# Optimization experiments

Hardware: AMD Instinct MI355X
Metric: run time of the kernel (lower is better)

## Reference

```python
import jax, jax.numpy as jnp
import numpy as np

N_RAYS = 131072
N_NODES = 524288
ENC_DEPTH = 8
ENC_DIM = 16
N_POINTS = 8
IN_DIM = N_POINTS * ENC_DEPTH * ENC_DIM  # 1024
INNER = 64


def setup_inputs() -> dict:
    key = jax.random.key(0)
    ks = jax.random.split(key, 9)
    orig = jax.random.uniform(ks[0], (N_RAYS, 3), dtype=jnp.float32)
    end = jax.random.uniform(ks[1], (N_RAYS, 3), dtype=jnp.float32)
    history = jax.random.randint(ks[2], (N_RAYS, ENC_DEPTH), 0, N_NODES, dtype=jnp.int32).astype(jnp.int64)
    nodes_min = jax.random.uniform(ks[3], (N_NODES, 3), dtype=jnp.float32)
    # extents strictly positive (module replaces 0 extents with 0.5)
    nodes_extent = jax.random.uniform(ks[4], (N_NODES, 3), dtype=jnp.float32) + 0.1
    emb = jax.random.normal(ks[5], (N_NODES, 8 * ENC_DIM), dtype=jnp.float32) * 0.1
    W1 = jax.random.normal(ks[6], (IN_DIM, INNER), dtype=jnp.float32) * (1.0 / np.sqrt(IN_DIM))
    W2 = jax.random.normal(ks[7], (INNER, INNER), dtype=jnp.float32) * (1.0 / np.sqrt(INNER))
    W3 = jax.random.normal(ks[8], (INNER, 2), dtype=jnp.float32) * (1.0 / np.sqrt(INNER))
    return {"orig": orig, "end": end, "history": history, "nodes_min": nodes_min,
            "nodes_extent": nodes_extent, "emb": emb, "W1": W1, "W2": W2, "W3": W3}


def _net_forward(orig, end, history, nodes_min, nodes_extent, emb, W1, W2, W3):
    n = orig.shape[0]
    d = history.shape[1]
    # gather per-ray, per-depth node data (irregular access)
    nmin = nodes_min[history]          # (n, d, 3)
    ext = nodes_extent[history]        # (n, d, 3)
    po = jnp.clip((orig[:, None, :] - nmin) / ext, 0.0, 1.0)  # (n, d, 3)
    pe = jnp.clip((end[:, None, :] - nmin) / ext, 0.0, 1.0)
    ts = jnp.linspace(0.0, 1.0, N_POINTS, dtype=orig.dtype)
    pts = po[:, :, None, :] + (pe - po)[:, :, None, :] * ts[None, None, :, None]  # (n, d, P, 3)
    xd, yd, zd = pts[..., 0], pts[..., 1], pts[..., 2]
    # corner weights in the same order as bbox_feature.chunk(8): 000,100,010,001,101,011,110,111
    w = jnp.stack([
        (1 - xd) * (1 - yd) * (1 - zd),
        xd * (1 - yd) * (1 - zd),
        (1 - xd) * yd * (1 - zd),
        (1 - xd) * (1 - yd) * zd,
        xd * (1 - yd) * zd,
        (1 - xd) * yd * zd,
        xd * yd * (1 - zd),
        xd * yd * zd,
    ], axis=-1)                                    # (n, d, P, 8)
    corners = emb[history].reshape(n, d, 8, ENC_DIM)  # (n, d, 8, F)
    feat = jnp.einsum('ndpk,ndkf->ndpf', w, corners)  # (n, d, P, F)
    feat = feat.reshape(n, d * N_POINTS * ENC_DIM)    # concat over depth
    h = jax.nn.relu(feat @ W1)
    h = jax.nn.relu(h @ W2)
    a = h @ W3                                        # (n, 2)
    lengths = jnp.linalg.norm(end - orig, axis=-1)
    pred_cls = a[:, 0]
    pred_dist = a[:, 1] * lengths
    return jnp.stack([pred_cls, pred_dist], axis=-1)  # (n, 2)


def reference(orig, end, history, nodes_min, nodes_extent, emb, W1, W2, W3):
    return _net_forward(orig, end, history, nodes_min, nodes_extent, emb, W1, W2, W3)
```

## Files before the change

### kernel.cpp

```cpp
#include <hip/hip_runtime.h>
#include <hip/hip_bf16.h>
#include <cstdint>

#define ENC_DEPTH 8
#define RAYS_PER_BLOCK 64
#define THREADS 512

typedef __attribute__((ext_vector_type(8))) short bf16x8;
typedef __attribute__((ext_vector_type(4))) float f32x4;

__device__ __forceinline__ unsigned short f2bf(float x) {
    union { float f; unsigned u; } v; v.f = x;
    unsigned r = v.u + 0x7fffu + ((v.u >> 16) & 1u);
    return (unsigned short)(r >> 16);
}
__device__ __forceinline__ float bf2f(unsigned short h) {
    union { unsigned u; float f; } v; v.u = ((unsigned)h) << 16;
    return v.f;
}
__device__ __forceinline__ float clamp01(float x) {
    return fminf(fmaxf(x, 0.0f), 1.0f);
}

__global__ __launch_bounds__(THREADS, 4) void nbvh_kernel(
    const float* __restrict__ orig, const float* __restrict__ endp,
    const int* __restrict__ hist, const float* __restrict__ nodes_min,
    const float* __restrict__ nodes_extent, const float* __restrict__ emb,
    const float* __restrict__ W1, const float* __restrict__ W2,
    const float* __restrict__ W3, float* __restrict__ out)
{
    __shared__ int hist_s[RAYS_PER_BLOCK * ENC_DEPTH];
    __shared__ float oe_s[RAYS_PER_BLOCK * 6];
    __shared__ __align__(16) unsigned short corners_s[RAYS_PER_BLOCK * 136];
    __shared__ __align__(16) unsigned short feat_s[RAYS_PER_BLOCK * 144];
    __shared__ __align__(16) unsigned short w1t_s[64 * 144];
    __shared__ float h1_s[RAYS_PER_BLOCK * 65];

    const int t = threadIdx.x;
    const int r0 = blockIdx.x * RAYS_PER_BLOCK;
    const int wave = t >> 6;
    const int lane = t & 63;

    hist_s[t] = hist[r0 * ENC_DEPTH + t];
    if (t < RAYS_PER_BLOCK * 3) {
        int ray = t / 3, c = t - ray * 3;
        oe_s[ray * 6 + c]     = orig[(r0 + ray) * 3 + c];
        oe_s[ray * 6 + 3 + c] = endp[(r0 + ray) * 3 + c];
    }

    f32x4 acc0 = {0.f, 0.f, 0.f, 0.f};
    f32x4 acc1 = {0.f, 0.f, 0.f, 0.f};
    const int m0 = (wave >> 1) * 16;
    const int n0 = (wave & 1) * 32;

    __syncthreads();

    for (int d = 0; d < ENC_DEPTH; ++d) {
        {
            int ray = t >> 3, k = t & 7;
            int node = hist_s[(ray << 3) + d];
            const float4* ep = (const float4*)(emb + ((size_t)node << 7) + (k << 4));
            float4 e0 = ep[0], e1 = ep[1], e2 = ep[2], e3 = ep[3];
            float e[16];
            e[0]=e0.x; e[1]=e0.y; e[2]=e0.z; e[3]=e0.w;
            e[4]=e1.x; e[5]=e1.y; e[6]=e1.z; e[7]=e1.w;
            e[8]=e2.x; e[9]=e2.y; e[10]=e2.z; e[11]=e2.w;
            e[12]=e3.x; e[13]=e3.y; e[14]=e3.z; e[15]=e3.w;
            unsigned short* cb = corners_s + ray * 136 + k;
            #pragma unroll
            for (int f = 0; f < 16; ++f) cb[f << 3] = f2bf(e[f]);
        }
        {
            int rl = t >> 2, cg = (t & 3) << 4;
            const float4* wp = (const float4*)(W1 + (size_t)(d * 128 + rl) * 64 + cg);
            float4 a0v = wp[0], a1v = wp[1], a2v = wp[2], a3v = wp[3];
            float a[16];
            a[0]=a0v.x; a[1]=a0v.y; a[2]=a0v.z; a[3]=a0v.w;
            a[4]=a1v.x; a[5]=a1v.y; a[6]=a1v.z; a[7]=a1v.w;
            a[8]=a2v.x; a[9]=a2v.y; a[10]=a2v.z; a[11]=a2v.w;
            a[12]=a3v.x; a[13]=a3v.y; a[14]=a3v.z; a[15]=a3v.w;
            unsigned short* wb = w1t_s + (size_t)cg * 144 + rl;
            #pragma unroll
            for (int i = 0; i < 16; ++i) wb[i * 144] = f2bf(a[i]);
        }
        __syncthreads();

        {
            int ray = t >> 3, p = t & 7;
            int node = hist_s[(ray << 3) + d];
            float nm0 = nodes_min[node * 3 + 0];
            float nm1 = nodes_min[node * 3 + 1];
            float nm2 = nodes_min[node * 3 + 2];
            float ex0 = nodes_extent[node * 3 + 0];
            float ex1 = nodes_extent[node * 3 + 1];
            float ex2 = nodes_extent[node * 3 + 2];
            const float* oe = oe_s + ray * 6;
            float po0 = clamp01((oe[0] - nm0) / ex0);
            float po1 = clamp01((oe[1] - nm1) / ex1);
            float po2 = clamp01((oe[2] - nm2) / ex2);
            float pe0 = clamp01((oe[3] - nm0) / ex0);
            float pe1 = clamp01((oe[4] - nm1) / ex1);
            float pe2 = clamp01((oe[5] - nm2) / ex2);
            float tt = (float)p * (1.0f / 7.0f);
            float x = po0 + (pe0 - po0) * tt;
            float y = po1 + (pe1 - po1) * tt;
            float z = po2 + (pe2 - po2) * tt;
            float ox = 1.f - x, oy = 1.f - y, oz = 1.f - z;
            float w[8];
            w[0] = ox * oy * oz;  w[1] = x * oy * oz;
            w[2] = ox * y * oz;   w[3] = ox * oy * z;
            w[4] = x * oy * z;    w[5] = ox * y * z;
            w[6] = x * y * oz;    w[7] = x * y * z;
            const unsigned short* cbase = corners_s + ray * 136;
            unsigned short* fb = feat_s + ray * 144 + (p << 4);
            #pragma unroll
            for (int f = 0; f < 16; ++f) {
                bf16x8 cv = *(const bf16x8*)(cbase + (f << 3));
                float acc = 0.f;
                #pragma unroll
                for (int k = 0; k < 8; ++k)
                    acc = fmaf(w[k], bf2f((unsigned short)cv[k]), acc);
                fb[f] = f2bf(acc);
            }
        }
        __syncthreads();

        {
            int q = lane >> 4, c = lane & 15;
            #pragma unroll
            for (int kk = 0; kk < 4; ++kk) {
                int koff = kk * 32 + q * 8;
                bf16x8 af = *(const bf16x8*)(feat_s + (m0 + c) * 144 + koff);
                bf16x8 b0 = *(const bf16x8*)(w1t_s + (n0 + c) * 144 + koff);
                bf16x8 b1 = *(const bf16x8*)(w1t_s + (n0 + 16 + c) * 144 + koff);
                acc0 = __builtin_amdgcn_mfma_f32_16x16x32_bf16(af, b0, acc0, 0, 0, 0);
                acc1 = __builtin_amdgcn_mfma_f32_16x16x32_bf16(af, b1, acc1, 0, 0, 0);
            }
        }
        __syncthreads();
    }

    {
        int colb = lane & 15, rq = (lane >> 4) << 2;
        #pragma unroll
        for (int r = 0; r < 4; ++r) {
            h1_s[(m0 + rq + r) * 65 + n0 + colb]      = fmaxf(acc0[r], 0.f);
            h1_s[(m0 + rq + r) * 65 + n0 + 16 + colb] = fmaxf(acc1[r], 0.f);
        }
    }
    __syncthreads();

    float* h2_s = (float*)corners_s;
    {
        int ray = t >> 3, jg = (t & 7) << 3;
        float s[8];
        #pragma unroll
        for (int j = 0; j < 8; ++j) s[j] = 0.f;
        const float* hrow = h1_s + ray * 65;
        #pragma unroll 8
        for (int i = 0; i < 64; ++i) {
            float hv = hrow[i];
            const float4* wr = (const float4*)(W2 + (i << 6) + jg);
            float4 wa = wr[0], wb = wr[1];
            s[0] = fmaf(hv, wa.x, s[0]); s[1] = fmaf(hv, wa.y, s[1]);
            s[2] = fmaf(hv, wa.z, s[2]); s[3] = fmaf(hv, wa.w, s[3]);
            s[4] = fmaf(hv, wb.x, s[4]); s[5] = fmaf(hv, wb.y, s[5]);
            s[6] = fmaf(hv, wb.z, s[6]); s[7] = fmaf(hv, wb.w, s[7]);
        }
        float* hb = h2_s + ray * 66 + jg;
        #pragma unroll
        for (int j = 0; j < 8; ++j) hb[j] = fmaxf(s[j], 0.f);
    }
    __syncthreads();

    if (t < 128) {
        int ray = t >> 1, c = t & 1;
        const float* hrow = h2_s + ray * 66;
        float a = 0.f;
        #pragma unroll 16
        for (int i = 0; i < 64; ++i) a = fmaf(hrow[i], W3[i * 2 + c], a);
        if (c) {
            const float* oe = oe_s + ray * 6;
            float dx = oe[3] - oe[0], dy = oe[4] - oe[1], dz = oe[5] - oe[2];
            a *= sqrtf(dx * dx + dy * dy + dz * dz);
        }
        out[((r0 + ray) << 1) + c] = a;
    }
}

extern "C" void kernel_launch(void* const* d_in, const int* in_sizes, int n_in,
                              void* d_out, int out_size, void* d_ws, size_t ws_size,
                              hipStream_t stream) {
    const float* orig = (const float*)d_in[0];
    const float* endp = (const float*)d_in[1];
    const int*   hist = (const int*)d_in[2];
    const float* nmin = (const float*)d_in[3];
    const float* next = (const float*)d_in[4];
    const float* emb  = (const float*)d_in[5];
    const float* W1   = (const float*)d_in[6];
    const float* W2   = (const float*)d_in[7];
    const float* W3   = (const float*)d_in[8];
    float* out = (float*)d_out;
    const int n_rays = in_sizes[0] / 3;
    dim3 grid(n_rays / RAYS_PER_BLOCK);
    nbvh_kernel<<<grid, THREADS, 0, stream>>>(orig, endp, hist, nmin, next,
                                              emb, W1, W2, W3, out);
}
```

Before: 533.3 us.

## Software-pipeline emb/W1/node gathers across depth and cut barriers per iteration

Prefetches the next depth's embedding corners, W1 slice and node bounds into registers while the current depth is processed. Barriers drop from three to two per iteration by merging the corner/W1 store phase with the weight computation. Barriers are now raw s_barrier calls with manual lgkmcnt waits instead of __syncthreads. Division becomes a hardware reciprocal, feature stores become vectorised 16-byte writes, and the LDS row stride goes from 144 to 136. The prefetch costs extra registers and may reduce occupancy, and the raw barriers leave vmem waits to the compiler.

```diff
diff --git a/kernel.cpp b/kernel.cpp
--- a/kernel.cpp
+++ b/kernel.cpp
@@ -32,14 +32,16 @@
     __shared__ int hist_s[RAYS_PER_BLOCK * ENC_DEPTH];
     __shared__ float oe_s[RAYS_PER_BLOCK * 6];
     __shared__ __align__(16) unsigned short corners_s[RAYS_PER_BLOCK * 136];
-    __shared__ __align__(16) unsigned short feat_s[RAYS_PER_BLOCK * 144];
-    __shared__ __align__(16) unsigned short w1t_s[64 * 144];
+    __shared__ __align__(16) unsigned short feat_s[RAYS_PER_BLOCK * 136];
+    __shared__ __align__(16) unsigned short w1t_s[64 * 136];
     __shared__ float h1_s[RAYS_PER_BLOCK * 65];
 
     const int t = threadIdx.x;
     const int r0 = blockIdx.x * RAYS_PER_BLOCK;
     const int wave = t >> 6;
     const int lane = t & 63;
+    const int ray_c = t >> 3, k_c = t & 7;
+    const int rl = t >> 2, cg = (t & 3) << 4;
 
     hist_s[t] = hist[r0 * ENC_DEPTH + t];
     if (t < RAYS_PER_BLOCK * 3) {
@@ -47,61 +49,77 @@
         oe_s[ray * 6 + c]     = orig[(r0 + ray) * 3 + c];
         oe_s[ray * 6 + 3 + c] = endp[(r0 + ray) * 3 + c];
     }
+    asm volatile("s_waitcnt lgkmcnt(0)" ::: "memory");
+
+    int node0 = hist_s[ray_c << 3];
+    const float4* ep = (const float4*)(emb + ((size_t)node0 << 7) + (k_c << 4));
+    float4 pf0 = ep[0], pf1 = ep[1], pf2 = ep[2], pf3 = ep[3];
+    const float4* wp = (const float4*)(W1 + (size_t)rl * 64 + cg);
+    float4 wf0 = wp[0], wf1 = wp[1], wf2 = wp[2], wf3 = wp[3];
+    float nm0 = nodes_min[node0 * 3 + 0];
+    float nm1 = nodes_min[node0 * 3 + 1];
+    float nm2 = nodes_min[node0 * 3 + 2];
+    float ex0 = nodes_extent[node0 * 3 + 0];
+    float ex1 = nodes_extent[node0 * 3 + 1];
+    float ex2 = nodes_extent[node0 * 3 + 2];
 
     f32x4 acc0 = {0.f, 0.f, 0.f, 0.f};
     f32x4 acc1 = {0.f, 0.f, 0.f, 0.f};
     const int m0 = (wave >> 1) * 16;
     const int n0 = (wave & 1) * 32;
 
-    __syncthreads();
+    __builtin_amdgcn_s_barrier();
+    asm volatile("" ::: "memory");
+
+    float nn0 = 0.f, nn1 = 0.f, nn2 = 0.f, en0 = 0.f, en1 = 0.f, en2 = 0.f;
 
     for (int d = 0; d < ENC_DEPTH; ++d) {
         {
-            int ray = t >> 3, k = t & 7;
-            int node = hist_s[(ray << 3) + d];
-            const float4* ep = (const float4*)(emb + ((size_t)node << 7) + (k << 4));
-            float4 e0 = ep[0], e1 = ep[1], e2 = ep[2], e3 = ep[3];
             float e[16];
-            e[0]=e0.x; e[1]=e0.y; e[2]=e0.z; e[3]=e0.w;
-            e[4]=e1.x; e[5]=e1.y; e[6]=e1.z; e[7]=e1.w;
-            e[8]=e2.x; e[9]=e2.y; e[10]=e2.z; e[11]=e2.w;
-            e[12]=e3.x; e[13]=e3.y; e[14]=e3.z; e[15]=e3.w;
-            unsigned short* cb = corners_s + ray * 136 + k;
+            e[0]=pf0.x; e[1]=pf0.y; e[2]=pf0.z; e[3]=pf0.w;
+            e[4]=pf1.x; e[5]=pf1.y; e[6]=pf1.z; e[7]=pf1.w;
+            e[8]=pf2.x; e[9]=pf2.y; e[10]=pf2.z; e[11]=pf2.w;
+            e[12]=pf3.x; e[13]=pf3.y; e[14]=pf3.z; e[15]=pf3.w;
+            unsigned short* cb = corners_s + ray_c * 136 + k_c;
             #pragma unroll
             for (int f = 0; f < 16; ++f) cb[f << 3] = f2bf(e[f]);
         }
         {
-            int rl = t >> 2, cg = (t & 3) << 4;
-            const float4* wp = (const float4*)(W1 + (size_t)(d * 128 + rl) * 64 + cg);
-            float4 a0v = wp[0], a1v = wp[1], a2v = wp[2], a3v = wp[3];
             float a[16];
-            a[0]=a0v.x; a[1]=a0v.y; a[2]=a0v.z; a[3]=a0v.w;
-            a[4]=a1v.x; a[5]=a1v.y; a[6]=a1v.z; a[7]=a1v.w;
-            a[8]=a2v.x; a[9]=a2v.y; a[10]=a2v.z; a[11]=a2v.w;
-            a[12]=a3v.x; a[13]=a3v.y; a[14]=a3v.z; a[15]=a3v.w;
-            unsigned short* wb = w1t_s + (size_t)cg * 144 + rl;
-            #pragma unroll
-            for (int i = 0; i < 16; ++i) wb[i * 144] = f2bf(a[i]);
-        }
-        __syncthreads();
-
-        {
-            int ray = t >> 3, p = t & 7;
-            int node = hist_s[(ray << 3) + d];
-            float nm0 = nodes_min[node * 3 + 0];
-            float nm1 = nodes_min[node * 3 + 1];
-            float nm2 = nodes_min[node * 3 + 2];
-            float ex0 = nodes_extent[node * 3 + 0];
-            float ex1 = nodes_extent[node * 3 + 1];
-            float ex2 = nodes_extent[node * 3 + 2];
-            const float* oe = oe_s + ray * 6;
-            float po0 = clamp01((oe[0] - nm0) / ex0);
-            float po1 = clamp01((oe[1] - nm1) / ex1);
-            float po2 = clamp01((oe[2] - nm2) / ex2);
-            float pe0 = clamp01((oe[3] - nm0) / ex0);
-            float pe1 = clamp01((oe[4] - nm1) / ex1);
-            float pe2 = clamp01((oe[5] - nm2) / ex2);
-            float tt = (float)p * (1.0f / 7.0f);
+            a[0]=wf0.x; a[1]=wf0.y; a[2]=wf0.z; a[3]=wf0.w;
+            a[4]=wf1.x; a[5]=wf1.y; a[6]=wf1.z; a[7]=wf1.w;
+            a[8]=wf2.x; a[9]=wf2.y; a[10]=wf2.z; a[11]=wf2.w;
+            a[12]=wf3.x; a[13]=wf3.y; a[14]=wf3.z; a[15]=wf3.w;
+            unsigned short* wb = w1t_s + (size_t)cg * 136 + rl;
+            #pragma unroll
+            for (int i = 0; i < 16; ++i) wb[i * 136] = f2bf(a[i]);
+        }
+        if (d < ENC_DEPTH - 1) {
+            int node1 = hist_s[(ray_c << 3) + d + 1];
+            const float4* ep2 = (const float4*)(emb + ((size_t)node1 << 7) + (k_c << 4));
+            pf0 = ep2[0]; pf1 = ep2[1]; pf2 = ep2[2]; pf3 = ep2[3];
+            const float4* wp2 = (const float4*)(W1 + (size_t)((d + 1) * 128 + rl) * 64 + cg);
+            wf0 = wp2[0]; wf1 = wp2[1]; wf2 = wp2[2]; wf3 = wp2[3];
+            nn0 = nodes_min[node1 * 3 + 0];
+            nn1 = nodes_min[node1 * 3 + 1];
+            nn2 = nodes_min[node1 * 3 + 2];
+            en0 = nodes_extent[node1 * 3 + 0];
+            en1 = nodes_extent[node1 * 3 + 1];
+            en2 = nodes_extent[node1 * 3 + 2];
+        }
+
+        {
+            const float* oe = oe_s + ray_c * 6;
+            float rx = __builtin_amdgcn_rcpf(ex0);
+            float ry = __builtin_amdgcn_rcpf(ex1);
+            float rz = __builtin_amdgcn_rcpf(ex2);
+            float po0 = clamp01((oe[0] - nm0) * rx);
+            float po1 = clamp01((oe[1] - nm1) * ry);
+            float po2 = clamp01((oe[2] - nm2) * rz);
+            float pe0 = clamp01((oe[3] - nm0) * rx);
+            float pe1 = clamp01((oe[4] - nm1) * ry);
+            float pe2 = clamp01((oe[5] - nm2) * rz);
+            float tt = (float)k_c * (1.0f / 7.0f);
             float x = po0 + (pe0 - po0) * tt;
             float y = po1 + (pe1 - po1) * tt;
             float z = po2 + (pe2 - po2) * tt;
@@ -111,8 +129,8 @@
             w[2] = ox * y * oz;   w[3] = ox * oy * z;
             w[4] = x * oy * z;    w[5] = ox * y * z;
             w[6] = x * y * oz;    w[7] = x * y * z;
-            const unsigned short* cbase = corners_s + ray * 136;
-            unsigned short* fb = feat_s + ray * 144 + (p << 4);
+            const unsigned short* cbase = corners_s + ray_c * 136;
+            bf16x8 f0v, f1v;
             #pragma unroll
             for (int f = 0; f < 16; ++f) {
                 bf16x8 cv = *(const bf16x8*)(cbase + (f << 3));
@@ -120,24 +138,39 @@
                 #pragma unroll
                 for (int k = 0; k < 8; ++k)
                     acc = fmaf(w[k], bf2f((unsigned short)cv[k]), acc);
-                fb[f] = f2bf(acc);
+                unsigned short h = f2bf(acc);
+                if (f < 8) f0v[f] = (short)h; else f1v[f - 8] = (short)h;
             }
-        }
-        __syncthreads();
+            unsigned short* fb = feat_s + ray_c * 136 + (k_c << 4);
+            *(bf16x8*)fb = f0v;
+            *(bf16x8*)(fb + 8) = f1v;
+        }
+
+        asm volatile("s_waitcnt lgkmcnt(0)" ::: "memory");
+        __builtin_amdgcn_s_barrier();
+        asm volatile("" ::: "memory");
 
         {
             int q = lane >> 4, c = lane & 15;
             #pragma unroll
             for (int kk = 0; kk < 4; ++kk) {
                 int koff = kk * 32 + q * 8;
-                bf16x8 af = *(const bf16x8*)(feat_s + (m0 + c) * 144 + koff);
-                bf16x8 b0 = *(const bf16x8*)(w1t_s + (n0 + c) * 144 + koff);
-                bf16x8 b1 = *(const bf16x8*)(w1t_s + (n0 + 16 + c) * 144 + koff);
+                bf16x8 af = *(const bf16x8*)(feat_s + (m0 + c) * 136 + koff);
+                bf16x8 b0 = *(const bf16x8*)(w1t_s + (n0 + c) * 136 + koff);
+                bf16x8 b1 = *(const bf16x8*)(w1t_s + (n0 + 16 + c) * 136 + koff);
                 acc0 = __builtin_amdgcn_mfma_f32_16x16x32_bf16(af, b0, acc0, 0, 0, 0);
                 acc1 = __builtin_amdgcn_mfma_f32_16x16x32_bf16(af, b1, acc1, 0, 0, 0);
             }
         }
-        __syncthreads();
+
+        asm volatile("s_waitcnt lgkmcnt(0)" ::: "memory");
+        __builtin_amdgcn_s_barrier();
+        asm volatile("" ::: "memory");
+
+        if (d < ENC_DEPTH - 1) {
+            nm0 = nn0; nm1 = nn1; nm2 = nn2;
+            ex0 = en0; ex1 = en1; ex2 = en2;
+        }
     }
 
     {
```

Result: no change. 539.3 us (+1.1%).
